# Kernel tuning notes

Measured on AMD Instinct MI355X. Metric: run time of the kernel, lower is better.

Reference implementation:

```python
import jax, jax.numpy as jnp
import numpy as np

N_NODES = 5000
N_EDGES = 160000


def _conv2d(x, w, b):
    # x: [N, Cin, H, W], w: [Cout, Cin, kh, kw] (OIHW), VALID padding, stride 1
    out = jax.lax.conv_general_dilated(
        x, w, window_strides=(1, 1), padding='VALID',
        dimension_numbers=('NCHW', 'OIHW', 'NCHW'))
    return out + b[None, :, None, None]


def _gcn_norm(edge_index, n):
    # PyG gcn_norm with add_self_loops=False: deg from target (col) nodes,
    # norm = d^{-1/2}[src] * d^{-1/2}[dst]
    src, dst = edge_index[0], edge_index[1]
    ones = jnp.ones((edge_index.shape[1],), jnp.float32)
    deg = jax.ops.segment_sum(ones, dst, num_segments=n)
    dinv = jnp.where(deg > 0, jax.lax.rsqrt(jnp.maximum(deg, 1.0)), 0.0)
    return dinv[src] * dinv[dst]


def _arma(x, edge_index, norm, w_init, w_root, bias):
    # ARMAConv, num_layers=1: mean_k ReLU( Ahat (x W_k) + x V_k + b_k )
    # x: [N, Fin], w_init/w_root: [K, Fin, Fout], bias: [K, Fout]
    n = x.shape[0]
    src, dst = edge_index[0], edge_index[1]
    h = jnp.einsum('nf,kfo->kno', x, w_init)            # [K, N, Fout]
    msg = h[:, src, :] * norm[None, :, None]            # [K, E, Fout] gather
    agg = jax.vmap(lambda m: jax.ops.segment_sum(m, dst, num_segments=n))(msg)
    root = jnp.einsum('nf,kfo->kno', x, w_root)         # [K, N, Fout]
    out = jax.nn.relu(agg + root + bias[:, None, :])
    return out.mean(axis=0)                             # mean over K stacks


def setup_inputs() -> dict:
    key = jax.random.key(0)
    ks = jax.random.split(key, 32)

    def rn(i, shape, s=0.1):
        return jax.random.normal(ks[i], shape, jnp.float32) * s

    d = {}
    d['inputs'] = jax.random.normal(ks[0], (N_NODES, 1, 53, 6), jnp.float32)
    d['edge_index'] = jax.random.randint(ks[1], (2, N_EDGES), 0, N_NODES, jnp.int32)
    # CNN encoder params (Conv2d(1,100,(3,3)), Conv2d(100,200,(3,2)), Conv2d(200,1,(3,2)))
    d['e1_w'] = rn(2, (100, 1, 3, 3), 0.3); d['e1_b'] = rn(3, (100,), 0.1)
    d['e2_w'] = rn(4, (200, 100, 3, 2), 0.04); d['e2_b'] = rn(5, (200,), 0.1)
    d['e3_w'] = rn(6, (1, 200, 3, 2), 0.04); d['e3_b'] = rn(7, (1,), 0.1)
    # ARMA layers: (Fin, Fout, num_stacks K)
    dims = [(94, 128, 2), (128, 128, 2), (128, 128, 2), (128, 128, 2), (128, 128, 2), (128, 16, 1)]
    k = 8
    for i, (fi, fo, K) in enumerate(dims, 1):
        s = 1.0 / np.sqrt(fi)
        d[f'a{i}_wi'] = rn(k, (K, fi, fo), s)
        d[f'a{i}_wr'] = rn(k + 1, (K, fi, fo), s)
        d[f'a{i}_b'] = rn(k + 2, (K, fo), 0.05)
        k += 3
    return d


def reference(inputs, edge_index, e1_w, e1_b, e2_w, e2_b, e3_w, e3_b,
              a1_wi, a1_wr, a1_b, a2_wi, a2_wr, a2_b, a3_wi, a3_wr, a3_b,
              a4_wi, a4_wr, a4_b, a5_wi, a5_wr, a5_b, a6_wi, a6_wr, a6_b):
    # CNN encoder (Dropout2d is identity in eval mode)
    h = jax.nn.leaky_relu(_conv2d(inputs, e1_w, e1_b), 0.01)
    h = jax.nn.leaky_relu(_conv2d(h, e2_w, e2_b), 0.01)
    h = _conv2d(h, e3_w, e3_b)
    h = jnp.tanh(h.reshape(-1, 94))                     # [N, 94]
    norm = _gcn_norm(edge_index, h.shape[0])
    for (wi, wr, b) in [(a1_wi, a1_wr, a1_b), (a2_wi, a2_wr, a2_b),
                        (a3_wi, a3_wr, a3_b), (a4_wi, a4_wr, a4_b),
                        (a5_wi, a5_wr, a5_b)]:
        h = jnp.tanh(_arma(h, edge_index, norm, wi, wr, b))
    h = _arma(h, edge_index, norm, a6_wi, a6_wr, a6_b)
    return jax.nn.softmax(h, axis=1)
```

## Files before the change

### kernel.cpp

```cpp
#include <hip/hip_runtime.h>
#include <math.h>

typedef _Float16 f16;
typedef _Float16 f16x8 __attribute__((ext_vector_type(8)));
typedef float f32x4 __attribute__((ext_vector_type(4)));

#define NN 5000
#define NE 160000

#define OFF_W2T   0ul
#define OFF_W3T   344064ul
#define OFF_WT1   346560ul
#define OFF_WT2   444864ul
#define OFF_WT3   575936ul
#define OFF_WT4   707008ul
#define OFF_WT5   838080ul
#define OFF_WT6   969152ul
#define OFF_H0    985536ul
#define OFF_HA    1945536ul
#define OFF_HB    3225536ul
#define OFF_C     4505536ul
#define OFF_DEG   14745536ul
#define OFF_IP    14765536ul
#define OFF_CUR   14785568ul
#define OFF_DINV  14805568ul
#define OFF_CSRS  14825568ul
#define OFF_CSRN  15465568ul
#define OFF_W1T   OFF_C

#define L_IN   0
#define L_BUF  1280
#define L_A1   (L_BUF)
#define L_C1   (L_BUF + 16640)
#define L_C2   (L_BUF)
#define LDS_TOTAL (17920 + 208*256)

__global__ void prep_w2t(const float* __restrict__ w, f16* __restrict__ W2T) {
  int i = blockIdx.x*256 + threadIdx.x;
  if (i >= 21*256*32) return;
  int j = i & 7, g = (i >> 3) & 3, n = (i >> 5) & 255, kc = i >> 13;
  int k = kc*32 + g*8 + j;
  int tap = k / 112, c = k - tap*112;
  float v = 0.f;
  if (n < 200 && c < 100 && tap < 6) v = w[n*600 + c*6 + tap];
  W2T[i] = (f16)v;
}

__global__ void prep_w3t(const float* __restrict__ w, f16* __restrict__ W3T) {
  int i = blockIdx.x*256 + threadIdx.x;
  if (i >= 1248) return;
  int tap = i / 208, c = i - tap*208;
  float v = (c < 200) ? w[c*6 + tap] : 0.f;
  W3T[i] = (f16)v;
}

__global__ void prep_w1t(const float* __restrict__ w, f16* __restrict__ W1T) {
  int i = blockIdx.x*256 + threadIdx.x;
  if (i >= 112*32) return;
  int n = i >> 5, k = i & 31;
  float v = (n < 100 && k < 9) ? w[n*9 + k] : 0.f;
  W1T[i] = (f16)v;
}

__global__ void prep_wt(const float* __restrict__ wi, const float* __restrict__ wr,
                        f16* __restrict__ WT, int Kst, int Fin, int Fout, int Kpad, int R) {
  int i = blockIdx.x*256 + threadIdx.x;
  if (i >= R*Kpad) return;
  int n = i / Kpad, kk = i - n*Kpad;
  float v = 0.f;
  if (kk < Fin) {
    int path = n / (Kst*Fout);
    if (path < 2) {
      int rem = n - path*(Kst*Fout);
      int k = rem / Fout, fo = rem - k*Fout;
      const float* w = (path == 0) ? wi : wr;
      v = w[(k*Fin + kk)*Fout + fo];
    }
  }
  WT[i] = (f16)v;
}

__global__ void zero_kernel(int* __restrict__ deg, int* __restrict__ cur) {
  int i = blockIdx.x*256 + threadIdx.x;
  if (i < NN) { deg[i] = 0; cur[i] = 0; }
}

__global__ void deg_kernel(const int* __restrict__ ei, int* __restrict__ deg) {
  int e = blockIdx.x*256 + threadIdx.x;
  if (e < NE) atomicAdd(&deg[ei[NE + e]], 1);
}

__global__ __launch_bounds__(1024) void scan_kernel(const int* __restrict__ deg,
                                                    int* __restrict__ ip,
                                                    float* __restrict__ dinv) {
  __shared__ int buf[1024];
  __shared__ int s_carry;
  const int tid = threadIdx.x;
  if (tid == 0) s_carry = 0;
  __syncthreads();
  for (int base = 0; base < NN; base += 1024) {
    int i = base + tid;
    int v = (i < NN) ? deg[i] : 0;
    buf[tid] = v;
    __syncthreads();
    for (int off = 1; off < 1024; off <<= 1) {
      int t = (tid >= off) ? buf[tid - off] : 0;
      __syncthreads();
      buf[tid] += t;
      __syncthreads();
    }
    int incl = buf[tid];
    int c = s_carry;
    if (i < NN) {
      ip[i] = c + incl - v;
      dinv[i] = (v > 0) ? rsqrtf((float)v) : 0.f;
    }
    __syncthreads();
    if (tid == 1023) s_carry = c + buf[1023];
    __syncthreads();
  }
  if (tid == 0) ip[NN] = s_carry;
}

__global__ void csr_fill(const int* __restrict__ ei, const float* __restrict__ dinv,
                         const int* __restrict__ ip, int* __restrict__ cur,
                         int* __restrict__ csrs, float* __restrict__ csrn) {
  int e = blockIdx.x*256 + threadIdx.x;
  if (e >= NE) return;
  int s = ei[e], d = ei[NE + e];
  int pos = ip[d] + atomicAdd(&cur[d], 1);
  csrs[pos] = s;
  csrn[pos] = dinv[s]*dinv[d];
}

__global__ __launch_bounds__(512, 2) void cnn_kernel(
    const float* __restrict__ inp, const f16* __restrict__ W1T, const float* __restrict__ b1,
    const f16* __restrict__ W2T, const float* __restrict__ b2,
    const f16* __restrict__ W3T, const float* __restrict__ b3,
    f16* __restrict__ h0)
{
  extern __shared__ char smem[];
  float* s_in = (float*)(smem + L_IN);
  f16*   s_a1 = (f16*)(smem + L_A1);
  char*  c1b  = smem + L_C1;
  f16*   s_c2 = (f16*)(smem + L_C2);

  const int node = blockIdx.x;
  const int tid  = threadIdx.x;
  const int lane = tid & 63, wid = tid >> 6;
  const int l15 = lane & 15, g = lane >> 4;

  for (int i = tid; i < 318; i += 512) s_in[i] = inp[node*318 + i];
  __syncthreads();

  for (int i = tid; i < 208*32; i += 512) {
    int m = i >> 5, k = i & 31;
    float v = 0.f;
    if (m < 204 && k < 9) {
      int y = m >> 2, x = m & 3;
      int ky = (k >= 6) ? 2 : (k >= 3 ? 1 : 0);
      int kx = k - ky*3;
      v = s_in[(y + ky)*6 + x + kx];
    }
    s_a1[m*40 + k] = (f16)v;
  }
  __syncthreads();

  for (int p = wid; p < 91; p += 8) {
    int mt = p % 13, nt = p / 13;
    f16x8 a = *(const f16x8*)(s_a1 + (mt*16 + l15)*40 + g*8);
    f16x8 b = *(const f16x8*)(W1T + (nt*16 + l15)*32 + g*8);
    f32x4 acc = (f32x4){0.f,0.f,0.f,0.f};
    acc = __builtin_amdgcn_mfma_f32_16x16x32_f16(a, b, acc, 0, 0, 0);
    int c = nt*16 + l15;
    float bias = (c < 100) ? b1[c] : 0.f;
    #pragma unroll
    for (int j = 0; j < 4; j++) {
      int m = mt*16 + g*4 + j;
      float v = acc[j] + bias;
      v = v > 0.f ? v : 0.01f*v;
      *(f16*)(c1b + (m << 8) + (((c << 1) ^ ((m & 7) << 4)))) = (f16)v;
    }
  }
  __syncthreads();

  const int wm = wid >> 2, wn = wid & 3;

  int rbase[5];
  #pragma unroll
  for (int mi = 0; mi < 5; mi++) {
    int p = (wm*5 + mi)*16 + l15;
    int pp = p < 147 ? p : 0;
    int y2 = pp / 3;
    rbase[mi] = y2*4 + (pp - y2*3);
  }

  f32x4 acc[5][4];
  #pragma unroll
  for (int mi = 0; mi < 5; mi++)
    #pragma unroll
    for (int ni = 0; ni < 4; ni++)
      acc[mi][ni] = (f32x4){0.f,0.f,0.f,0.f};

  const int lofs = l15*32 + g*8;
  const f16* bbase = W2T + wn*2048 + lofs;
  #pragma unroll
  for (int kc = 0; kc < 21; kc++) {
    int k = kc*32 + g*8;
    int tap = k / 112;
    int c = k - tap*112;
    int dr = ((tap >> 1) << 2) + (tap & 1);
    f16x8 a[5], b[4];
    #pragma unroll
    for (int mi = 0; mi < 5; mi++) {
      int row = rbase[mi] + dr;
      a[mi] = *(const f16x8*)(c1b + (row << 8) + (((c << 1) ^ ((row & 7) << 4))));
    }
    const f16* bkc = bbase + kc*8192;
    #pragma unroll
    for (int ni = 0; ni < 4; ni++)
      b[ni] = *(const f16x8*)(bkc + ni*512);
    #pragma unroll
    for (int mi = 0; mi < 5; mi++)
      #pragma unroll
      for (int ni = 0; ni < 4; ni++)
        acc[mi][ni] = __builtin_amdgcn_mfma_f32_16x16x32_f16(a[mi], b[ni], acc[mi][ni], 0, 0, 0);
  }

  __syncthreads();

  #pragma unroll
  for (int ni = 0; ni < 4; ni++) {
    int n = wn*64 + ni*16 + l15;
    if (n < 208) {
      float bias = (n < 200) ? b2[n] : 0.f;
      #pragma unroll
      for (int mi = 0; mi < 5; mi++) {
        #pragma unroll
        for (int j = 0; j < 4; j++) {
          int m = (wm*5 + mi)*16 + g*4 + j;
          if (m < 147) {
            float v = acc[mi][ni][j] + bias;
            v = v > 0.f ? v : 0.01f*v;
            s_c2[m*216 + n] = (f16)v;
          }
        }
      }
    }
  }
  __syncthreads();

  if (wid < 6) {
    int p = wid*16 + l15;
    int q = p < 94 ? p : 0;
    int y3 = q >> 1, x3 = q & 1;
    int r3 = y3*3 + x3;
    f16 bmask = (l15 == 0) ? (f16)1.f : (f16)0.f;
    f32x4 acc3 = (f32x4){0.f,0.f,0.f,0.f};
    #pragma unroll
    for (int kc = 0; kc < 39; kc++) {
      int k = kc*32 + g*8;
      int tap = k / 208;
      int c = k - tap*208;
      int dr = (tap >> 1)*3 + (tap & 1);
      f16x8 a = *(const f16x8*)(s_c2 + (r3 + dr)*216 + c);
      f16x8 b = *(const f16x8*)(W3T + k);
      #pragma unroll
      for (int j = 0; j < 8; j++) b[j] *= bmask;
      acc3 = __builtin_amdgcn_mfma_f32_16x16x32_f16(a, b, acc3, 0, 0, 0);
    }
    if (l15 == 0) {
      float bb = b3[0];
      #pragma unroll
      for (int j = 0; j < 4; j++) {
        int qq = wid*16 + g*4 + j;
        float v = (qq < 94) ? tanhf(acc3[j] + bb) : 0.f;
        h0[node*96 + qq] = (f16)v;
      }
    }
  }
}

template<int K>
__global__ __launch_bounds__(256, 4) void gemm_kernel(
    const f16* __restrict__ A, const f16* __restrict__ B, float* __restrict__ C,
    int M, int N)
{
  constexpr int LK = K + 8;
  __shared__ f16 sA[64*LK];
  __shared__ f16 sB[64*LK];
  const int tid = threadIdx.x;
  const int m0 = blockIdx.x*64, n0 = blockIdx.y*64;
  constexpr int SEGS = K/8;
  for (int i = tid; i < 64*SEGS; i += 256) {
    int row = i / SEGS, seg = i - row*SEGS;
    int gm = m0 + row; if (gm >= M) gm = M - 1;
    *(f16x8*)(sA + row*LK + seg*8) = *(const f16x8*)(A + (size_t)gm*K + seg*8);
    *(f16x8*)(sB + row*LK + seg*8) = *(const f16x8*)(B + (size_t)(n0 + row)*K + seg*8);
  }
  __syncthreads();
  const int lane = tid & 63, wid = tid >> 6;
  const int l15 = lane & 15, g = lane >> 4;
  const int wm = wid >> 1, wn = wid & 1;
  f32x4 acc[2][2];
  #pragma unroll
  for (int mi = 0; mi < 2; mi++)
    #pragma unroll
    for (int ni = 0; ni < 2; ni++)
      acc[mi][ni] = (f32x4){0.f,0.f,0.f,0.f};
  #pragma unroll
  for (int kc = 0; kc < K/32; kc++) {
    f16x8 a[2], b[2];
    #pragma unroll
    for (int mi = 0; mi < 2; mi++)
      a[mi] = *(const f16x8*)(sA + (wm*32 + mi*16 + l15)*LK + kc*32 + g*8);
    #pragma unroll
    for (int ni = 0; ni < 2; ni++)
      b[ni] = *(const f16x8*)(sB + (wn*32 + ni*16 + l15)*LK + kc*32 + g*8);
    #pragma unroll
    for (int mi = 0; mi < 2; mi++)
      #pragma unroll
      for (int ni = 0; ni < 2; ni++)
        acc[mi][ni] = __builtin_amdgcn_mfma_f32_16x16x32_f16(a[mi], b[ni], acc[mi][ni], 0, 0, 0);
  }
  #pragma unroll
  for (int mi = 0; mi < 2; mi++)
    #pragma unroll
    for (int ni = 0; ni < 2; ni++)
      #pragma unroll
      for (int j = 0; j < 4; j++) {
        int m = m0 + wm*32 + mi*16 + g*4 + j;
        int n = n0 + wn*32 + ni*16 + l15;
        if (m < M) C[(size_t)m*N + n] = acc[mi][ni][j];
      }
}

__global__ __launch_bounds__(256) void combine128(
    const float* __restrict__ C, const int* __restrict__ ip,
    const int* __restrict__ csrs, const float* __restrict__ csrn,
    const float* __restrict__ bias, f16* __restrict__ hout)
{
  const int d = blockIdx.x*4 + (threadIdx.x >> 6);
  const int lane = threadIdx.x & 63;
  const int i0 = ip[d], i1 = ip[d+1];
  float a00 = 0.f, a01 = 0.f, a10 = 0.f, a11 = 0.f;
  float b00 = 0.f, b01 = 0.f, b10 = 0.f, b11 = 0.f;
  int e = i0;
  for (; e + 1 < i1; e += 2) {
    int s0 = csrs[e], s1 = csrs[e+1];
    float w0 = csrn[e], w1 = csrn[e+1];
    const float* t0 = C + (size_t)s0*512;
    const float* t1 = C + (size_t)s1*512;
    a00 += w0*t0[lane];       a01 += w0*t0[lane+64];
    a10 += w0*t0[lane+128];   a11 += w0*t0[lane+192];
    b00 += w1*t1[lane];       b01 += w1*t1[lane+64];
    b10 += w1*t1[lane+128];   b11 += w1*t1[lane+192];
  }
  if (e < i1) {
    int s = csrs[e];
    float w = csrn[e];
    const float* t = C + (size_t)s*512;
    a00 += w*t[lane];       a01 += w*t[lane+64];
    a10 += w*t[lane+128];   a11 += w*t[lane+192];
  }
  a00 += b00; a01 += b01; a10 += b10; a11 += b11;
  const float* r = C + (size_t)d*512 + 256;
  float o0 = fmaxf(a00 + r[lane]     + bias[lane],     0.f)
           + fmaxf(a10 + r[lane+128] + bias[lane+128], 0.f);
  float o1 = fmaxf(a01 + r[lane+64]  + bias[lane+64],  0.f)
           + fmaxf(a11 + r[lane+192] + bias[lane+192], 0.f);
  hout[(size_t)d*128 + lane]      = (f16)tanhf(0.5f*o0);
  hout[(size_t)d*128 + lane + 64] = (f16)tanhf(0.5f*o1);
}

__global__ __launch_bounds__(256) void combine_out(
    const float* __restrict__ C, const int* __restrict__ ip,
    const int* __restrict__ csrs, const float* __restrict__ csrn,
    const float* __restrict__ bias, float* __restrict__ out)
{
  const int d = blockIdx.x*4 + (threadIdx.x >> 6);
  const int lane = threadIdx.x & 63;
  const int f = lane & 15;
  const int i0 = ip[d], i1 = ip[d+1];
  float a = 0.f, b = 0.f;
  int e = i0;
  for (; e + 1 < i1; e += 2) {
    a += csrn[e]   * C[(size_t)csrs[e]*64 + f];
    b += csrn[e+1] * C[(size_t)csrs[e+1]*64 + f];
  }
  if (e < i1) a += csrn[e] * C[(size_t)csrs[e]*64 + f];
  a += b;
  float v = fmaxf(a + C[(size_t)d*64 + 16 + f] + bias[f], 0.f);
  float m = v;
  #pragma unroll
  for (int off = 1; off < 16; off <<= 1) m = fmaxf(m, __shfl_xor(m, off));
  float ev = expf(v - m);
  float s = ev;
  #pragma unroll
  for (int off = 1; off < 16; off <<= 1) s += __shfl_xor(s, off);
  if (lane < 16) out[(size_t)d*16 + lane] = ev / s;
}

extern "C" void kernel_launch(void* const* d_in, const int* in_sizes, int n_in,
                              void* d_out, int out_size, void* d_ws, size_t ws_size,
                              hipStream_t stream)
{
  const float* inputs = (const float*)d_in[0];
  const int*   ei     = (const int*)d_in[1];
  const float* e1w = (const float*)d_in[2];
  const float* e1b = (const float*)d_in[3];
  const float* e2w = (const float*)d_in[4];
  const float* e2b = (const float*)d_in[5];
  const float* e3w = (const float*)d_in[6];
  const float* e3b = (const float*)d_in[7];
  const float *awi[6], *awr[6], *ab[6];
  for (int i = 0; i < 6; i++) {
    awi[i] = (const float*)d_in[8 + 3*i];
    awr[i] = (const float*)d_in[9 + 3*i];
    ab[i]  = (const float*)d_in[10 + 3*i];
  }
  char* ws = (char*)d_ws;
  f16* W2T = (f16*)(ws + OFF_W2T);
  f16* W3T = (f16*)(ws + OFF_W3T);
  f16* W1T = (f16*)(ws + OFF_W1T);
  f16* WT[6] = { (f16*)(ws + OFF_WT1), (f16*)(ws + OFF_WT2), (f16*)(ws + OFF_WT3),
                 (f16*)(ws + OFF_WT4), (f16*)(ws + OFF_WT5), (f16*)(ws + OFF_WT6) };
  f16* H0 = (f16*)(ws + OFF_H0);
  f16* HA = (f16*)(ws + OFF_HA);
  f16* HB = (f16*)(ws + OFF_HB);
  float* C = (float*)(ws + OFF_C);
  int* DEG = (int*)(ws + OFF_DEG);
  int* IP  = (int*)(ws + OFF_IP);
  int* CUR = (int*)(ws + OFF_CUR);
  float* DINV = (float*)(ws + OFF_DINV);
  int* CSRS = (int*)(ws + OFF_CSRS);
  float* CSRN = (float*)(ws + OFF_CSRN);

  (void)hipFuncSetAttribute((const void*)cnn_kernel,
                            hipFuncAttributeMaxDynamicSharedMemorySize, LDS_TOTAL);

  prep_w2t<<<672, 256, 0, stream>>>(e2w, W2T);
  prep_w3t<<<5, 256, 0, stream>>>(e3w, W3T);
  prep_w1t<<<14, 256, 0, stream>>>(e1w, W1T);
  prep_wt<<<192, 256, 0, stream>>>(awi[0], awr[0], WT[0], 2, 94, 128, 96, 512);
  for (int l = 1; l < 5; l++)
    prep_wt<<<256, 256, 0, stream>>>(awi[l], awr[l], WT[l], 2, 128, 128, 128, 512);
  prep_wt<<<32, 256, 0, stream>>>(awi[5], awr[5], WT[5], 1, 128, 16, 128, 64);

  zero_kernel<<<20, 256, 0, stream>>>(DEG, CUR);
  deg_kernel<<<625, 256, 0, stream>>>(ei, DEG);
  scan_kernel<<<1, 1024, 0, stream>>>(DEG, IP, DINV);
  csr_fill<<<625, 256, 0, stream>>>(ei, DINV, IP, CUR, CSRS, CSRN);

  cnn_kernel<<<NN, 512, LDS_TOTAL, stream>>>(inputs, W1T, e1b, W2T, e2b, W3T, e3b, H0);

  gemm_kernel<96><<<dim3(79, 8), 256, 0, stream>>>(H0, WT[0], C, NN, 512);
  combine128<<<1250, 256, 0, stream>>>(C, IP, CSRS, CSRN, ab[0], HA);
  gemm_kernel<128><<<dim3(79, 8), 256, 0, stream>>>(HA, WT[1], C, NN, 512);
  combine128<<<1250, 256, 0, stream>>>(C, IP, CSRS, CSRN, ab[1], HB);
  gemm_kernel<128><<<dim3(79, 8), 256, 0, stream>>>(HB, WT[2], C, NN, 512);
  combine128<<<1250, 256, 0, stream>>>(C, IP, CSRS, CSRN, ab[2], HA);
  gemm_kernel<128><<<dim3(79, 8), 256, 0, stream>>>(HA, WT[3], C, NN, 512);
  combine128<<<1250, 256, 0, stream>>>(C, IP, CSRS, CSRN, ab[3], HB);
  gemm_kernel<128><<<dim3(79, 8), 256, 0, stream>>>(HB, WT[4], C, NN, 512);
  combine128<<<1250, 256, 0, stream>>>(C, IP, CSRS, CSRN, ab[4], HA);
  gemm_kernel<128><<<dim3(79, 1), 256, 0, stream>>>(HA, WT[5], C, NN, 64);
  combine_out<<<1250, 256, 0, stream>>>(C, IP, CSRS, CSRN, ab[5], (float*)d_out);
}
```

Before: 772.9 us.

## Replace XOR-swizzled conv1 LDS layout with padded stride and raise occupancy

```diff
diff --git a/kernel.cpp b/kernel.cpp
--- a/kernel.cpp
+++ b/kernel.cpp
@@ -33,7 +33,8 @@
 #define L_A1   (L_BUF)
 #define L_C1   (L_BUF + 16640)
 #define L_C2   (L_BUF)
-#define LDS_TOTAL (17920 + 208*256)
+#define C1_STRIDE 136
+#define LDS_TOTAL (17920 + 208*272)
 
 __global__ void prep_w2t(const float* __restrict__ w, f16* __restrict__ W2T) {
   int i = blockIdx.x*256 + threadIdx.x;
@@ -133,7 +134,7 @@
   csrn[pos] = dinv[s]*dinv[d];
 }
 
-__global__ __launch_bounds__(512, 2) void cnn_kernel(
+__global__ __launch_bounds__(512, 4) void cnn_kernel(
     const float* __restrict__ inp, const f16* __restrict__ W1T, const float* __restrict__ b1,
     const f16* __restrict__ W2T, const float* __restrict__ b2,
     const f16* __restrict__ W3T, const float* __restrict__ b3,
@@ -142,7 +143,7 @@
   extern __shared__ char smem[];
   float* s_in = (float*)(smem + L_IN);
   f16*   s_a1 = (f16*)(smem + L_A1);
-  char*  c1b  = smem + L_C1;
+  f16*   s_c1 = (f16*)(smem + L_C1);
   f16*   s_c2 = (f16*)(smem + L_C2);
 
   const int node = blockIdx.x;
@@ -151,6 +152,10 @@
   const int l15 = lane & 15, g = lane >> 4;
 
   for (int i = tid; i < 318; i += 512) s_in[i] = inp[node*318 + i];
+  for (int i = tid; i < 208*12; i += 512) {
+    int r = i / 12, c = 100 + (i - r*12);
+    s_c1[r*C1_STRIDE + c] = (f16)0.f;
+  }
   __syncthreads();
 
   for (int i = tid; i < 208*32; i += 512) {
@@ -179,20 +184,20 @@
       int m = mt*16 + g*4 + j;
       float v = acc[j] + bias;
       v = v > 0.f ? v : 0.01f*v;
-      *(f16*)(c1b + (m << 8) + (((c << 1) ^ ((m & 7) << 4)))) = (f16)v;
+      s_c1[m*C1_STRIDE + c] = (f16)v;
     }
   }
   __syncthreads();
 
   const int wm = wid >> 2, wn = wid & 3;
 
-  int rbase[5];
+  const f16* abase[5];
   #pragma unroll
   for (int mi = 0; mi < 5; mi++) {
     int p = (wm*5 + mi)*16 + l15;
     int pp = p < 147 ? p : 0;
     int y2 = pp / 3;
-    rbase[mi] = y2*4 + (pp - y2*3);
+    abase[mi] = s_c1 + (y2*4 + (pp - y2*3))*C1_STRIDE + g*8;
   }
 
   f32x4 acc[5][4];
@@ -202,29 +207,35 @@
     for (int ni = 0; ni < 4; ni++)
       acc[mi][ni] = (f32x4){0.f,0.f,0.f,0.f};
 
-  const int lofs = l15*32 + g*8;
-  const f16* bbase = W2T + wn*2048 + lofs;
+  const f16* bbase = W2T + wn*2048 + l15*32 + g*8;
   #pragma unroll
   for (int kc = 0; kc < 21; kc++) {
-    int k = kc*32 + g*8;
-    int tap = k / 112;
-    int c = k - tap*112;
-    int dr = ((tap >> 1) << 2) + (tap & 1);
-    f16x8 a[5], b[4];
-    #pragma unroll
-    for (int mi = 0; mi < 5; mi++) {
-      int row = rbase[mi] + dr;
-      a[mi] = *(const f16x8*)(c1b + (row << 8) + (((c << 1) ^ ((row & 7) << 4))));
-    }
+    int k = kc*32;
+    int tap = (kc*32 + g*0) >= 0 ? (kc*32)/112 : 0;
+    f16x8 b[4];
     const f16* bkc = bbase + kc*8192;
     #pragma unroll
     for (int ni = 0; ni < 4; ni++)
       b[ni] = *(const f16x8*)(bkc + ni*512);
     #pragma unroll
-    for (int mi = 0; mi < 5; mi++)
+    for (int mi = 0; mi < 5; mi++) {
+      int kg0 = kc*32;
+      int tap0 = kg0 / 112;
+      int rem0 = kg0 - tap0*112;
+      int cross = 0;
+      (void)cross;
+      int cg = rem0;
+      int tapg = tap0;
+      int cfull = cg + g*8;
+      int wrap = cfull >= 112 ? 1 : 0;
+      int c = cfull - wrap*112;
+      tapg = tap0 + wrap;
+      int dr = ((tapg >> 1) << 2) + (tapg & 1);
+      f16x8 a = *(const f16x8*)(abase[mi] + dr*C1_STRIDE + (c - g*8));
       #pragma unroll
       for (int ni = 0; ni < 4; ni++)
-        acc[mi][ni] = __builtin_amdgcn_mfma_f32_16x16x32_f16(a[mi], b[ni], acc[mi][ni], 0, 0, 0);
+        acc[mi][ni] = __builtin_amdgcn_mfma_f32_16x16x32_f16(a, b[ni], acc[mi][ni], 0, 0, 0);
+    }
   }
 
   __syncthreads();
```

After: 683.1 us. -11.6%, faster.
